# Optimization experiments

Hardware: AMD Instinct MI355X
Metric: run time of the kernel (lower is better)

## Reference

```python
import jax, jax.numpy as jnp
import numpy as np
from jax.scipy.special import gammaln

PRIOR = 0.25      # downsample_rate -> Binomial prior on boundary frequency
TEMP = 1.0        # gumbel (RelaxedBernoulli) temperature
THRESHOLD = 0.5   # hard-boundary threshold

B, L, D = 8, 2048, 1024


def setup_inputs() -> dict:
    key = jax.random.key(0)
    k_x, k_u, k_w1, k_w2, k_ng = jax.random.split(key, 5)
    x = jax.random.normal(k_x, (B, L, D), dtype=jnp.float32)
    noise = jax.random.uniform(k_u, (B, L), dtype=jnp.float32)
    W1 = jax.random.normal(k_w1, (D, D), dtype=jnp.float32) / np.sqrt(D)
    b1 = jnp.zeros((D,), dtype=jnp.float32)
    W2 = jax.random.normal(k_w2, (D, 1), dtype=jnp.float32) / np.sqrt(D)
    b2 = jnp.zeros((1,), dtype=jnp.float32)
    null_group = jax.random.normal(k_ng, (1, 1, D), dtype=jnp.float32)
    return {"x": x, "noise": noise, "W1": W1, "b1": b1, "W2": W2, "b2": b2,
            "null_group": null_group}


def _common(boundaries, n_segments, upsample):
    # boundaries: [B, L] -> soft group-offset tensor foo: [B, L, S]
    hh1 = jnp.cumsum(boundaries, axis=1)
    if not upsample:
        hh1 = hh1 - boundaries
    s = jnp.arange(n_segments, dtype=boundaries.dtype)
    return s[None, None, :] - hh1[:, :, None]


def _final(foo, upsample):
    # indicator of token-l belonging to segment-s, normalized (mean-pool / gather)
    lel = jnp.where(foo != 0, 0.0, 1.0 - foo)
    axis = 2 if upsample else 1
    return lel / (jnp.sum(lel, axis=axis, keepdims=True) + 1e-9)


def reference(x, noise, W1, b1, W2, b2, null_group):
    Bn, Ln, Dn = x.shape
    S_max = Ln  # static upper bound on segment count (padded; extra segs = zeros)

    # --- boundary predictor (gumbel / RelaxedBernoulli rsample, temp=1) ---
    logits = (jax.nn.relu(x @ W1 + b1) @ W2 + b2)[..., 0]            # [B, L]
    u = jnp.clip(noise, 1e-6, 1.0 - 1e-6)
    soft = jax.nn.sigmoid((logits + jnp.log(u) - jnp.log1p(-u)) / TEMP)
    hard_val = (soft > THRESHOLD).astype(soft.dtype)
    hard = jax.lax.stop_gradient(hard_val - soft) + soft             # straight-through

    # --- downsample: mean-pool each variable-length segment ---
    bar_d = _final(_common(hard, S_max, False), False)               # [B, L, S]
    pooled = jnp.einsum('bld,bls->bsd', x, bar_d)                    # [B, S, D]
    shortened = jnp.concatenate(
        [jnp.broadcast_to(null_group, (Bn, 1, Dn)), pooled], axis=1)  # [B, S+1, D]

    # --- upsample: token l reads segment cumsum(hard)[l] (null group = 0) ---
    bar_u = _final(_common(hard, S_max + 1, True), True)             # [B, L, S+1]
    upsampled = jnp.einsum('bsd,bls->bld', shortened, bar_u)         # [B, L, D]

    # --- consistency loss: -log Binomial(L, prior).pmf(#boundaries) / L ---
    k = jnp.sum(hard, axis=-1)                                       # [B]
    Lf = jnp.asarray(Ln, soft.dtype)
    logp = (gammaln(Lf + 1.0) - gammaln(k + 1.0) - gammaln(Lf - k + 1.0)
            + k * jnp.log(PRIOR) + (Lf - k) * jnp.log1p(-PRIOR))
    loss = -jnp.mean(logp) / Ln

    return shortened, upsampled, loss
```

## Files before the change

### kernel.cpp

```cpp
#include <hip/hip_runtime.h>
#include <math.h>

#define Bq 8
#define Lq 2048
#define Dq 1024
#define Mq (Bq*Lq)
#define Sq 2048
#define SP1 2049
#define FLAG_CAP 8192
#define MARGIN 0.06f

typedef __attribute__((ext_vector_type(8))) short short8;
typedef __attribute__((ext_vector_type(4))) float f32x4;

static __device__ __forceinline__ ushort f2bf(float f) {
  union { float f; uint32_t u; } v; v.f = f;
  uint32_t u = v.u;
  return (ushort)((u + 0x7FFF + ((u >> 16) & 1)) >> 16);
}

static __device__ __forceinline__ void gload_lds16(const void* gsrc, void* lds) {
  __builtin_amdgcn_global_load_lds(
      (const __attribute__((address_space(1))) uint32_t*)(uintptr_t)gsrc,
      (__attribute__((address_space(3))) uint32_t*)(uint32_t)(uintptr_t)lds,
      16, 0, 0);
}

__global__ void init_logits(float* __restrict__ logits, const float* __restrict__ b2,
                            int* __restrict__ count) {
  int i = blockIdx.x * 256 + threadIdx.x;
  if (i < Mq) logits[i] = b2[0];
  if (i == 0) *count = 0;
}

__global__ void convert_x(const float* __restrict__ x, ushort* __restrict__ xb) {
  int i = blockIdx.x * 256 + threadIdx.x;
  float4 v = ((const float4*)x)[i];
  ushort4 o;
  o.x = f2bf(v.x); o.y = f2bf(v.y); o.z = f2bf(v.z); o.w = f2bf(v.w);
  ((ushort4*)xb)[i] = o;
}

__global__ void convert_w1t(const float* __restrict__ W1, ushort* __restrict__ Wt) {
  __shared__ ushort sh[32][33];
  const int tx = threadIdx.x & 31, ty = threadIdx.x >> 5;
  const int k0 = blockIdx.x * 32, n0 = blockIdx.y * 32;
  #pragma unroll
  for (int r = 0; r < 32; r += 8)
    sh[ty + r][tx] = f2bf(W1[(size_t)(k0 + ty + r) * Dq + n0 + tx]);
  __syncthreads();
  #pragma unroll
  for (int r = 0; r < 32; r += 8)
    Wt[(size_t)(n0 + ty + r) * Dq + k0 + tx] = sh[tx][ty + r];
}

__global__ __launch_bounds__(256) void mfma_gemm(
    const ushort* __restrict__ Xb,
    const ushort* __restrict__ Wt,
    const float* __restrict__ b1, const float* __restrict__ W2,
    float* __restrict__ logits)
{
  __shared__ ushort Al[128 * 32];
  __shared__ ushort Bl[128 * 32];
  __shared__ float red[128];
  const int tid = threadIdx.x;
  const int w = tid >> 6, lane = tid & 63;
  const int m0 = blockIdx.x * 128, n0 = blockIdx.y * 128;
  const int wr = w >> 1, wc = w & 1;
  const int lr = lane & 15, lq = lane >> 4;

  f32x4 acc[4][4] = {};
  if (tid < 128) red[tid] = 0.f;

  for (int kt = 0; kt < Dq; kt += 32) {
    #pragma unroll
    for (int s = 0; s < 2; ++s) {
      int rbase = s * 64 + w * 16;
      const ushort* srcA = Xb + (size_t)(m0 + rbase + (lane >> 2)) * Dq + kt + (lane & 3) * 8;
      gload_lds16(srcA, &Al[rbase * 32]);
      const ushort* srcB = Wt + (size_t)(n0 + rbase + (lane >> 2)) * Dq + kt + (lane & 3) * 8;
      gload_lds16(srcB, &Bl[rbase * 32]);
    }
    __syncthreads();
    short8 a[4], b[4];
    #pragma unroll
    for (int m = 0; m < 4; ++m)
      a[m] = *(const short8*)&Al[(wr * 64 + m * 16 + lr) * 32 + lq * 8];
    #pragma unroll
    for (int n = 0; n < 4; ++n)
      b[n] = *(const short8*)&Bl[(wc * 64 + n * 16 + lr) * 32 + lq * 8];
    #pragma unroll
    for (int m = 0; m < 4; ++m)
      #pragma unroll
      for (int n = 0; n < 4; ++n)
        acc[m][n] = __builtin_amdgcn_mfma_f32_16x16x32_bf16(a[m], b[n], acc[m][n], 0, 0, 0);
    __syncthreads();
  }

  float q[4][4];
  #pragma unroll
  for (int m = 0; m < 4; ++m)
    #pragma unroll
    for (int r = 0; r < 4; ++r) q[m][r] = 0.f;
  #pragma unroll
  for (int n = 0; n < 4; ++n) {
    int col = n0 + wc * 64 + n * 16 + lr;
    float bb = b1[col];
    float ww = W2[col];
    #pragma unroll
    for (int m = 0; m < 4; ++m)
      #pragma unroll
      for (int r = 0; r < 4; ++r) {
        float v = acc[m][n][r] + bb;
        v = v > 0.f ? v : 0.f;
        q[m][r] = fmaf(v, ww, q[m][r]);
      }
  }
  #pragma unroll
  for (int m = 0; m < 4; ++m)
    #pragma unroll
    for (int r = 0; r < 4; ++r) {
      float s = q[m][r];
      s += __shfl_xor(s, 1); s += __shfl_xor(s, 2);
      s += __shfl_xor(s, 4); s += __shfl_xor(s, 8);
      if (lr == 0) atomicAdd(&red[wr * 64 + m * 16 + lq * 4 + r], s);
    }
  __syncthreads();
  if (tid < 128) atomicAdd(&logits[m0 + tid], red[tid]);
}

__global__ void flag_kernel(const float* __restrict__ logits, const float* __restrict__ noise,
                            int* __restrict__ count, int* __restrict__ list) {
  int i = blockIdx.x * 256 + threadIdx.x;
  float u = noise[i];
  u = fminf(fmaxf(u, 1e-6f), 0.999999f);
  float z = (logits[i] + logf(u)) - log1pf(-u);
  if (fabsf(z) < MARGIN) {
    int id = atomicAdd(count, 1);
    if (id < FLAG_CAP) list[id] = i;
  }
}

__global__ void gather_kernel(const float* __restrict__ x, const int* __restrict__ count,
                              const int* __restrict__ list, const float* __restrict__ b2,
                              float* __restrict__ Abuf, float* __restrict__ logits) {
  int cnt = *count; if (cnt > FLAG_CAP) cnt = FLAG_CAP;
  if (cnt <= 0) return;
  float b2v = b2[0];
  for (int f = blockIdx.x; f < cnt; f += gridDim.x) {
    int tok = list[f];
    ((float4*)(Abuf + (size_t)f * Dq))[threadIdx.x] =
        ((const float4*)(x + (size_t)tok * Dq))[threadIdx.x];
    if (threadIdx.x == 0) logits[tok] = b2v;
  }
}

__global__ __launch_bounds__(256) void fix_gemm(
    const float* __restrict__ Abuf, const float* __restrict__ W1,
    const float* __restrict__ b1, const float* __restrict__ W2,
    const int* __restrict__ count, const int* __restrict__ list,
    float* __restrict__ logits)
{
  __shared__ float Asl[32][33];
  __shared__ float Bsl[32][128];
  int cnt = *count; if (cnt > FLAG_CAP) cnt = FLAG_CAP;
  if (cnt <= 0) return;
  int tiles_m = (cnt + 31) >> 5;
  int total = tiles_m * 8;
  const int tid = threadIdx.x;
  const int tx = tid & 31, ty = tid >> 5;
  for (int t = blockIdx.x; t < total; t += gridDim.x) {
    int m0 = (t >> 3) * 32, n0 = (t & 7) * 128;
    float C[4][4] = {};
    for (int k0 = 0; k0 < Dq; k0 += 32) {
      __syncthreads();
      {
        int mr = tid >> 3, kf = tid & 7;
        float4 va = *(const float4*)(Abuf + (size_t)(m0 + mr) * Dq + k0 + kf * 4);
        Asl[kf*4+0][mr] = va.x; Asl[kf*4+1][mr] = va.y;
        Asl[kf*4+2][mr] = va.z; Asl[kf*4+3][mr] = va.w;
      }
      #pragma unroll
      for (int s = 0; s < 4; ++s) {
        int slot = tid + s * 256;
        int kb = slot >> 5, nf = slot & 31;
        *(float4*)(&Bsl[kb][nf*4]) =
            *(const float4*)(W1 + (size_t)(k0 + kb) * Dq + n0 + nf * 4);
      }
      __syncthreads();
      #pragma unroll
      for (int k = 0; k < 32; ++k) {
        float a[4], b[4];
        #pragma unroll
        for (int i = 0; i < 4; ++i) a[i] = Asl[k][ty*4+i];
        #pragma unroll
        for (int j = 0; j < 4; ++j) b[j] = Bsl[k][tx + 32*j];
        #pragma unroll
        for (int i = 0; i < 4; ++i)
          #pragma unroll
          for (int j = 0; j < 4; ++j)
            C[i][j] = fmaf(a[i], b[j], C[i][j]);
      }
    }
    float p[4] = {0,0,0,0};
    #pragma unroll
    for (int j = 0; j < 4; ++j) {
      int gn = n0 + tx + 32*j;
      float bb = b1[gn], ww = W2[gn];
      #pragma unroll
      for (int i = 0; i < 4; ++i) {
        float v = C[i][j] + bb; v = v > 0.f ? v : 0.f;
        p[i] = fmaf(v, ww, p[i]);
      }
    }
    #pragma unroll
    for (int i = 0; i < 4; ++i) {
      float s = p[i];
      s += __shfl_xor(s, 1); s += __shfl_xor(s, 2); s += __shfl_xor(s, 4);
      s += __shfl_xor(s, 8); s += __shfl_xor(s, 16);
      int m = m0 + ty*4 + i;
      if (tx == 0 && m < cnt) atomicAdd(&logits[list[m]], s);
    }
    __syncthreads();
  }
}

__global__ __launch_bounds__(256) void boundary_scan(
    const float* __restrict__ logits, const float* __restrict__ noise,
    int* __restrict__ segup, int* __restrict__ starts, int* __restrict__ ends,
    int* __restrict__ nsegs, int* __restrict__ kb)
{
  const int b = blockIdx.x;
  const int t = threadIdx.x;
  __shared__ unsigned char sh_hard[Lq];
  __shared__ int wsum[4];
  const int l0 = t * 8;
  int h[8];
  int localsum = 0;
  #pragma unroll
  for (int j = 0; j < 8; ++j) {
    int l = l0 + j;
    float u = noise[b * Lq + l];
    u = fminf(fmaxf(u, 1e-6f), 0.999999f);
    float z = (logits[b * Lq + l] + logf(u)) - log1pf(-u);
    int hd = (z > 0.f) ? 1 : 0;
    h[j] = hd;
    sh_hard[l] = (unsigned char)hd;
    localsum += hd;
  }
  int lane = t & 63, w = t >> 6;
  int v = localsum;
  #pragma unroll
  for (int off = 1; off < 64; off <<= 1) {
    int n = __shfl_up(v, off);
    if (lane >= off) v += n;
  }
  if (lane == 63) wsum[w] = v;
  __syncthreads();
  int wpre = 0;
  for (int i = 0; i < w; ++i) wpre += wsum[i];
  int run = wpre + (v - localsum);
  #pragma unroll
  for (int j = 0; j < 8; ++j) {
    int l = l0 + j;
    run += h[j];
    segup[b * Lq + l] = run;
    int sd = run - h[j];
    int hp = (l == 0) ? 1 : (int)sh_hard[l - 1];
    if (hp) starts[b * Sq + sd] = l;
    if (h[j] || l == Lq - 1) ends[b * Sq + sd] = l + 1;
    if (l == Lq - 1) { nsegs[b] = sd + 1; kb[b] = run; }
  }
}

__global__ __launch_bounds__(256) void pool_kernel(
    const float* __restrict__ x, const float* __restrict__ null_group,
    const int* __restrict__ starts, const int* __restrict__ ends,
    const int* __restrict__ nsegs, float* __restrict__ outS)
{
  const int so = blockIdx.x;
  const int b  = blockIdx.y;
  const int d4 = threadIdx.x;
  float4* dst = (float4*)(outS + ((size_t)b * SP1 + so) * Dq) + d4;
  if (so == 0) { *dst = ((const float4*)null_group)[d4]; return; }
  int s = so - 1;
  if (s >= nsegs[b]) { float4 z; z.x = z.y = z.z = z.w = 0.f; *dst = z; return; }
  int st = starts[b * Sq + s], en = ends[b * Sq + s];
  float4 acc; acc.x = acc.y = acc.z = acc.w = 0.f;
  for (int l = st; l < en; ++l) {
    float4 vv = ((const float4*)(x + ((size_t)b * Lq + l) * Dq))[d4];
    acc.x += vv.x; acc.y += vv.y; acc.z += vv.z; acc.w += vv.w;
  }
  float inv = 1.f / (float)(en - st);
  acc.x *= inv; acc.y *= inv; acc.z *= inv; acc.w *= inv;
  *dst = acc;
}

__global__ __launch_bounds__(256) void upsample_kernel(
    const float* __restrict__ outS, const int* __restrict__ segup,
    float* __restrict__ outU)
{
  const int l = blockIdx.x, b = blockIdx.y;
  const int d4 = threadIdx.x;
  int sg = segup[b * Lq + l];
  ((float4*)(outU + ((size_t)b * Lq + l) * Dq))[d4] =
      ((const float4*)(outS + ((size_t)b * SP1 + sg) * Dq))[d4];
}

__global__ void loss_kernel(const int* __restrict__ kb, float* __restrict__ out)
{
  int t = threadIdx.x;
  float lp = 0.f;
  if (t < Bq) {
    float k  = (float)kb[t];
    float Lf = (float)Lq;
    lp = lgammaf(Lf + 1.f) - lgammaf(k + 1.f) - lgammaf(Lf - k + 1.f)
       + k * logf(0.25f) + (Lf - k) * log1pf(-0.25f);
  }
  #pragma unroll
  for (int off = 32; off > 0; off >>= 1) lp += __shfl_down(lp, off);
  if (t == 0) out[0] = -(lp / (float)Bq) / (float)Lq;
}

extern "C" void kernel_launch(void* const* d_in, const int* in_sizes, int n_in,
                              void* d_out, int out_size, void* d_ws, size_t ws_size,
                              hipStream_t stream) {
  const float* x     = (const float*)d_in[0];
  const float* noise = (const float*)d_in[1];
  const float* W1    = (const float*)d_in[2];
  const float* b1    = (const float*)d_in[3];
  const float* W2    = (const float*)d_in[4];
  const float* b2    = (const float*)d_in[5];
  const float* ng    = (const float*)d_in[6];

  float* outS = (float*)d_out;
  float* outU = outS + (size_t)Bq * SP1 * Dq;
  float* outL = outU + (size_t)Bq * Lq * Dq;

  ushort* xb   = (ushort*)outU;
  ushort* wt   = (ushort*)((char*)outU + (size_t)33554432);
  float*  Abuf = outS;

  char* ws = (char*)d_ws;
  float* logits = (float*)(ws);
  int*   segup  = (int*)(ws + 65536);
  int*   starts = (int*)(ws + 131072);
  int*   ends   = (int*)(ws + 196608);
  int*   nsegs  = (int*)(ws + 262144);
  int*   kb     = (int*)(ws + 262400);
  int*   count  = (int*)(ws + 262656);
  int*   list   = (int*)(ws + 262912);

  init_logits<<<Mq / 256, 256, 0, stream>>>(logits, b2, count);
  convert_x<<<(Mq * Dq / 4) / 256, 256, 0, stream>>>(x, xb);
  convert_w1t<<<dim3(32, 32), 256, 0, stream>>>(W1, wt);
  mfma_gemm<<<dim3(Mq / 128, Dq / 128), 256, 0, stream>>>(xb, wt, b1, W2, logits);
  flag_kernel<<<Mq / 256, 256, 0, stream>>>(logits, noise, count, list);
  gather_kernel<<<512, 256, 0, stream>>>(x, count, list, b2, Abuf, logits);
  fix_gemm<<<1024, 256, 0, stream>>>(Abuf, W1, b1, W2, count, list, logits);
  boundary_scan<<<Bq, 256, 0, stream>>>(logits, noise, segup, starts, ends, nsegs, kb);
  pool_kernel<<<dim3(SP1, Bq), 256, 0, stream>>>(x, ng, starts, ends, nsegs, outS);
  upsample_kernel<<<dim3(Lq, Bq), 256, 0, stream>>>(outS, segup, outU);
  loss_kernel<<<1, 64, 0, stream>>>(kb, outL);
}
```

Measured before the change: 364.6 us.

## Split fp32 fix-up GEMM over K slices and gather rows directly

Near-threshold tokens were recomputed with an fp32 GEMM whose parallelism was limited by the small number of flagged rows. This change splits K into eight slices so more blocks can work at once. Partial hidden sums go to a scratch buffer, and a second kernel reduces them, applies bias, ReLU and W2, and writes the logits. The separate gather kernel is removed because rows are read from x through the flag list. FLAG_CAP drops from 8192 to 1024, which could silently drop flagged tokens if more than 1024 fall inside the margin.

Result: faster. 311.9 us (-14.5%).

```diff
diff --git a/kernel.cpp b/kernel.cpp
--- a/kernel.cpp
+++ b/kernel.cpp
@@ -7,7 +7,8 @@
 #define Mq (Bq*Lq)
 #define Sq 2048
 #define SP1 2049
-#define FLAG_CAP 8192
+#define FLAG_CAP 1024
+#define KSLICES 8
 #define MARGIN 0.06f
 
 typedef __attribute__((ext_vector_type(8))) short short8;
@@ -141,42 +142,32 @@
   }
 }
 
-__global__ void gather_kernel(const float* __restrict__ x, const int* __restrict__ count,
-                              const int* __restrict__ list, const float* __restrict__ b2,
-                              float* __restrict__ Abuf, float* __restrict__ logits) {
-  int cnt = *count; if (cnt > FLAG_CAP) cnt = FLAG_CAP;
-  if (cnt <= 0) return;
-  float b2v = b2[0];
-  for (int f = blockIdx.x; f < cnt; f += gridDim.x) {
-    int tok = list[f];
-    ((float4*)(Abuf + (size_t)f * Dq))[threadIdx.x] =
-        ((const float4*)(x + (size_t)tok * Dq))[threadIdx.x];
-    if (threadIdx.x == 0) logits[tok] = b2v;
-  }
-}
-
-__global__ __launch_bounds__(256) void fix_gemm(
-    const float* __restrict__ Abuf, const float* __restrict__ W1,
-    const float* __restrict__ b1, const float* __restrict__ W2,
+__global__ __launch_bounds__(256) void fix_part1(
+    const float* __restrict__ x, const float* __restrict__ W1,
     const int* __restrict__ count, const int* __restrict__ list,
-    float* __restrict__ logits)
+    float* __restrict__ hbuf)
 {
   __shared__ float Asl[32][33];
   __shared__ float Bsl[32][128];
   int cnt = *count; if (cnt > FLAG_CAP) cnt = FLAG_CAP;
   if (cnt <= 0) return;
   int tiles_m = (cnt + 31) >> 5;
-  int total = tiles_m * 8;
+  int total = tiles_m * 8 * KSLICES;
   const int tid = threadIdx.x;
   const int tx = tid & 31, ty = tid >> 5;
   for (int t = blockIdx.x; t < total; t += gridDim.x) {
-    int m0 = (t >> 3) * 32, n0 = (t & 7) * 128;
+    int m0 = (t / (8 * KSLICES)) * 32;
+    int n0 = ((t / KSLICES) & 7) * 128;
+    int kbase = (t % KSLICES) * (Dq / KSLICES);
     float C[4][4] = {};
-    for (int k0 = 0; k0 < Dq; k0 += 32) {
+    for (int kc = 0; kc < Dq / KSLICES; kc += 32) {
+      int k0 = kbase + kc;
       __syncthreads();
       {
         int mr = tid >> 3, kf = tid & 7;
-        float4 va = *(const float4*)(Abuf + (size_t)(m0 + mr) * Dq + k0 + kf * 4);
+        int fidx = m0 + mr; if (fidx >= cnt) fidx = cnt - 1;
+        int tok = list[fidx];
+        float4 va = *(const float4*)(x + (size_t)tok * Dq + k0 + kf * 4);
         Asl[kf*4+0][mr] = va.x; Asl[kf*4+1][mr] = va.y;
         Asl[kf*4+2][mr] = va.z; Asl[kf*4+3][mr] = va.w;
       }
@@ -202,25 +193,50 @@
             C[i][j] = fmaf(a[i], b[j], C[i][j]);
       }
     }
-    float p[4] = {0,0,0,0};
-    #pragma unroll
-    for (int j = 0; j < 4; ++j) {
-      int gn = n0 + tx + 32*j;
-      float bb = b1[gn], ww = W2[gn];
-      #pragma unroll
-      for (int i = 0; i < 4; ++i) {
-        float v = C[i][j] + bb; v = v > 0.f ? v : 0.f;
-        p[i] = fmaf(v, ww, p[i]);
-      }
-    }
+    int ks = t % KSLICES;
     #pragma unroll
     for (int i = 0; i < 4; ++i) {
-      float s = p[i];
-      s += __shfl_xor(s, 1); s += __shfl_xor(s, 2); s += __shfl_xor(s, 4);
-      s += __shfl_xor(s, 8); s += __shfl_xor(s, 16);
-      int m = m0 + ty*4 + i;
-      if (tx == 0 && m < cnt) atomicAdd(&logits[list[m]], s);
-    }
+      int f = m0 + ty*4 + i;
+      float* dst = hbuf + ((size_t)ks * FLAG_CAP + f) * Dq + n0 + tx;
+      #pragma unroll
+      for (int j = 0; j < 4; ++j) dst[32*j] = C[i][j];
+    }
+    __syncthreads();
+  }
+}
+
+__global__ __launch_bounds__(256) void fix_part2(
+    const float* __restrict__ hbuf, const float* __restrict__ b1,
+    const float* __restrict__ W2, const float* __restrict__ b2,
+    const int* __restrict__ count, const int* __restrict__ list,
+    float* __restrict__ logits)
+{
+  __shared__ float rs[4];
+  int cnt = *count; if (cnt > FLAG_CAP) cnt = FLAG_CAP;
+  const int tid = threadIdx.x;
+  const int lane = tid & 63, w = tid >> 6;
+  float b2v = b2[0];
+  for (int f = blockIdx.x; f < cnt; f += gridDim.x) {
+    int n = tid * 4;
+    float4 h = {0.f, 0.f, 0.f, 0.f};
+    #pragma unroll
+    for (int ks = 0; ks < KSLICES; ++ks) {
+      float4 pv = *(const float4*)(hbuf + ((size_t)ks * FLAG_CAP + f) * Dq + n);
+      h.x += pv.x; h.y += pv.y; h.z += pv.z; h.w += pv.w;
+    }
+    float4 bb = *(const float4*)(b1 + n);
+    float4 ww = *(const float4*)(W2 + n);
+    float p = 0.f;
+    float v;
+    v = h.x + bb.x; v = v > 0.f ? v : 0.f; p = fmaf(v, ww.x, p);
+    v = h.y + bb.y; v = v > 0.f ? v : 0.f; p = fmaf(v, ww.y, p);
+    v = h.z + bb.z; v = v > 0.f ? v : 0.f; p = fmaf(v, ww.z, p);
+    v = h.w + bb.w; v = v > 0.f ? v : 0.f; p = fmaf(v, ww.w, p);
+    #pragma unroll
+    for (int off = 32; off > 0; off >>= 1) p += __shfl_xor(p, off);
+    if (lane == 0) rs[w] = p;
+    __syncthreads();
+    if (tid == 0) logits[list[f]] = b2v + rs[0] + rs[1] + rs[2] + rs[3];
     __syncthreads();
   }
 }
@@ -339,7 +355,7 @@
 
   ushort* xb   = (ushort*)outU;
   ushort* wt   = (ushort*)((char*)outU + (size_t)33554432);
-  float*  Abuf = outS;
+  float*  hbuf = outS;
 
   char* ws = (char*)d_ws;
   float* logits = (float*)(ws);
@@ -356,8 +372,8 @@
   convert_w1t<<<dim3(32, 32), 256, 0, stream>>>(W1, wt);
   mfma_gemm<<<dim3(Mq / 128, Dq / 128), 256, 0, stream>>>(xb, wt, b1, W2, logits);
   flag_kernel<<<Mq / 256, 256, 0, stream>>>(logits, noise, count, list);
-  gather_kernel<<<512, 256, 0, stream>>>(x, count, list, b2, Abuf, logits);
-  fix_gemm<<<1024, 256, 0, stream>>>(Abuf, W1, b1, W2, count, list, logits);
+  fix_part1<<<2048, 256, 0, stream>>>(x, W1, count, list, hbuf);
+  fix_part2<<<1024, 256, 0, stream>>>(hbuf, b1, W2, b2, count, list, logits);
   boundary_scan<<<Bq, 256, 0, stream>>>(logits, noise, segup, starts, ends, nsegs, kb);
   pool_kernel<<<dim3(SP1, Bq), 256, 0, stream>>>(x, ng, starts, ends, nsegs, outS);
   upsample_kernel<<<dim3(Lq, Bq), 256, 0, stream>>>(outS, segup, outU);
```
